# Kernel optimization log

Hardware: AMD Instinct MI355X
Metric: run time of the kernel (lower is better)

Reference implementation:

```python
import jax, jax.numpy as jnp
import numpy as np

B, S_ENC, T_DEC, I, H = 1024, 49, 25, 76, 2048  # S_ENC = source_seq_len - 1


def setup_inputs() -> dict:
    key = jax.random.key(0)
    ks = jax.random.split(key, 6)
    sc = 0.02
    return {
        "encoder_inputs": jax.random.normal(ks[0], (B, S_ENC, I), jnp.float32),
        "decoder_inputs": jax.random.normal(ks[1], (B, T_DEC, I), jnp.float32),
        "W_ih": jax.random.normal(ks[2], (3 * H, I), jnp.float32) * sc,
        "W_hh": jax.random.normal(ks[3], (3 * H, H), jnp.float32) * sc,
        "b_ih": jnp.zeros((3 * H,), jnp.float32),
        "b_hh": jnp.zeros((3 * H,), jnp.float32),
        "fc_w": jax.random.normal(ks[4], (I, H), jnp.float32) * sc,
        "fc_b": jnp.zeros((I,), jnp.float32),
    }


def gru_cell(x, h, W_ih, W_hh, b_ih, b_hh):
    # PyTorch GRUCell: gates stacked [r; z; n] along first axis of weights.
    gi = x @ W_ih.T + b_ih  # [B, 3H]
    gh = h @ W_hh.T + b_hh  # [B, 3H]
    i_r, i_z, i_n = jnp.split(gi, 3, axis=-1)
    h_r, h_z, h_n = jnp.split(gh, 3, axis=-1)
    r = jax.nn.sigmoid(i_r + h_r)
    z = jax.nn.sigmoid(i_z + h_z)
    n = jnp.tanh(i_n + r * h_n)
    return (1.0 - z) * n + z * h


def reference(encoder_inputs, decoder_inputs, W_ih, W_hh, b_ih, b_hh, fc_w, fc_b):
    # Dropout p=0.0 (and eval mode) -> identity; omitted.
    h0 = jnp.zeros((encoder_inputs.shape[0], H), encoder_inputs.dtype)
    enc = jnp.swapaxes(encoder_inputs, 0, 1)  # [S_ENC, B, I]

    def enc_step(h, x):
        return gru_cell(x, h, W_ih, W_hh, b_ih, b_hh), None

    h, _ = jax.lax.scan(enc_step, h0, enc)

    # Sampling-based decoding: only decoder_inputs[:, 0] is consumed; every
    # later step feeds back the previous output. Each step's input is detached.
    prev0 = decoder_inputs[:, 0, :]

    def dec_step(carry, _):
        h, prev = carry
        inp = jax.lax.stop_gradient(prev)  # inp.detach() in the torch code
        h_new = gru_cell(inp, h, W_ih, W_hh, b_ih, b_hh)
        out = inp + h_new @ fc_w.T + fc_b  # residual over fc1 projection
        return (h_new, out), out

    _, outs = jax.lax.scan(dec_step, (h, prev0), None, length=T_DEC)
    return jnp.swapaxes(outs, 0, 1)  # [B, T_DEC, I]
```

## Files before the change

### kernel.cpp

```cpp
#include <hip/hip_runtime.h>
#include <cstdint>
#include <cstddef>

#define DI __device__ __forceinline__

typedef __bf16 bf16x8 __attribute__((ext_vector_type(8)));
typedef float  f32x4  __attribute__((ext_vector_type(4)));
typedef unsigned short ushort_t;

constexpr int BATCH = 1024;
constexpr int HID   = 2048;
constexpr int IN    = 76;
constexpr int SENC  = 49;
constexpr int TDEC  = 25;
constexpr int KX    = 128;
constexpr int KP    = KX + HID;
constexpr int BK    = 64;
constexpr int KTT   = KP / BK;
constexpr int OSTR  = TDEC * IN;

DI unsigned short f2bf(float f) {
  union { float f; unsigned u; } v; v.f = f;
  unsigned u = v.u;
  return (unsigned short)((u + 0x7fffu + ((u >> 16) & 1u)) >> 16);
}

DI float bf2f(unsigned short h) {
  union { unsigned u; float f; } v; v.u = ((unsigned)h) << 16;
  return v.f;
}

DI f32x4 mfma16(bf16x8 a, bf16x8 b, f32x4 c) {
  return __builtin_amdgcn_mfma_f32_16x16x32_bf16(a, b, c, 0, 0, 0);
}

DI void gload_lds16(const void* g, void* l) {
  __builtin_amdgcn_global_load_lds((const __attribute__((address_space(1))) void*)g,
                                   (__attribute__((address_space(3))) void*)l,
                                   16, 0, 0);
}

DI float sigmoidf_(float x) { return 1.0f / (1.0f + __expf(-x)); }
DI float tanhf_(float x)    { return 1.0f - 2.0f / (1.0f + __expf(2.0f * x)); }


__global__ void pack_W(const float* __restrict__ Wih, const float* __restrict__ Whh,
                       ushort_t* __restrict__ Wp) {
  int idx = blockIdx.x * 256 + threadIdx.x;
  if (idx >= 6144 * KP) return;
  int n = idx / KP;
  int k = idx - n * KP;
  float v = 0.f;
  if (k < IN)        v = Wih[(size_t)n * IN + k];
  else if (k >= KX)  v = Whh[(size_t)n * HID + (k - KX)];
  Wp[idx] = f2bf(v);
}

__global__ void pack_xe(const float* __restrict__ enc, ushort_t* __restrict__ xe) {
  int idx = blockIdx.x * 256 + threadIdx.x;
  if (idx >= SENC * BATCH * KX) return;
  int t = idx >> 17;
  int rem = idx & 131071;
  int b = rem >> 7, k = rem & 127;
  float v = (k < IN) ? enc[(size_t)b * (SENC * IN) + t * IN + k] : 0.f;
  xe[idx] = f2bf(v);
}

__global__ void pack_xd0(const float* __restrict__ dec, ushort_t* __restrict__ xd) {
  int idx = blockIdx.x * 256 + threadIdx.x;
  if (idx >= BATCH * KX) return;
  int b = idx >> 7, k = idx & 127;
  float v = (k < IN) ? dec[(size_t)b * OSTR + k] : 0.f;
  xd[idx] = f2bf(v);
}

__global__ void pack_fc(const float* __restrict__ fcw, ushort_t* __restrict__ Wfc) {
  int idx = blockIdx.x * 256 + threadIdx.x;
  if (idx >= 80 * HID) return;
  int n = idx >> 11, k = idx & 2047;
  float v = (n < IN) ? fcw[(size_t)n * HID + k] : 0.f;
  Wfc[idx] = f2bf(v);
}

__global__ __launch_bounds__(256, 2) void gru_step_kernel(
    const ushort_t* __restrict__ x,
    const ushort_t* __restrict__ hbp,
    const ushort_t* __restrict__ Wp,
    const float*    __restrict__ b_ih,
    const float*    __restrict__ b_hh,
    ushort_t*       __restrict__ hbn)
{
  __shared__ ushort_t lds[2][(128 + 96) * BK];

  const int tid  = threadIdx.x;
  const int lane = tid & 63;
  const int wid  = tid >> 6;
  const int bid  = blockIdx.x;
  const int xcd   = bid & 7;
  const int idx   = bid >> 3;
  const int m_grp = idx & 7;
  const int n_grp = xcd + 8 * (idx >> 3);
  const int row0  = m_grp * 128;
  const int col0  = n_grp * 32;
  const int wm = wid >> 1;
  const int wn = wid & 1;

  const f32x4 Z4 = {0.f, 0.f, 0.f, 0.f};
  f32x4 accr[4], accz[4], accN[4], accin[4];
  #pragma unroll
  for (int a = 0; a < 4; ++a) { accr[a] = Z4; accz[a] = Z4; accN[a] = Z4; accin[a] = Z4; }

  const int srow  = lane >> 3;
  const int swcol = (((lane & 7) ^ (srow & 7)) << 3);

  const int lr  = lane & 15;
  const int bc  = (lane >> 4) * 16;
  const int ksw0 = ((bc)      ^ ((lane & 7) << 4)) >> 1;
  const int ksw1 = ((64 + bc) ^ ((lane & 7) << 4)) >> 1;

  auto stage = [&](int buf, int kt) {
    const ushort_t* asrc; int astr, ak0;
    if (kt < 2) { asrc = x;   astr = KX;  ak0 = kt * BK; }
    else        { asrc = hbp; astr = HID; ak0 = (kt - 2) * BK; }
    ushort_t* Lb = &lds[buf][0];
    #pragma unroll
    for (int c = 0; c < 4; ++c) {
      const int chunk = wid * 4 + c;
      const ushort_t* g = asrc + (size_t)(row0 + chunk * 8 + srow) * astr + ak0 + swcol;
      gload_lds16(g, Lb + chunk * 512);
    }
    const int wk0 = kt * BK;
    #pragma unroll
    for (int c = 0; c < 3; ++c) {
      const int chunk = wid * 3 + c;
      const int brow = chunk * 8 + srow;
      const int gg = brow >> 5, wi = brow & 31;
      const ushort_t* g = Wp + (size_t)(gg * HID + col0 + wi) * KP + wk0 + swcol;
      gload_lds16(g, Lb + 128 * BK + chunk * 512);
    }
  };

  auto readFrags = [&](const ushort_t* base, int ko, bf16x8 af[4], bf16x8 bg[3]) {
    #pragma unroll
    for (int fm = 0; fm < 4; ++fm)
      af[fm] = *reinterpret_cast<const bf16x8*>(&base[(wm * 64 + fm * 16 + lr) * BK + ko]);
    #pragma unroll
    for (int g = 0; g < 3; ++g)
      bg[g] = *reinterpret_cast<const bf16x8*>(
          &base[128 * BK + (g * 32 + wn * 16 + lr) * BK + ko]);
  };

  auto burst = [&](bf16x8 af[4], bf16x8 bg[3]) {
    __builtin_amdgcn_s_setprio(1);
    #pragma unroll
    for (int fm = 0; fm < 4; ++fm) {
      accr[fm] = mfma16(af[fm], bg[0], accr[fm]);
      accz[fm] = mfma16(af[fm], bg[1], accz[fm]);
      accN[fm] = mfma16(af[fm], bg[2], accN[fm]);
    }
    __builtin_amdgcn_s_setprio(0);
  };

  bf16x8 afA[4], bgA[3];
  bf16x8 afB[4], bgB[3];

  stage(0, 0);
  asm volatile("s_waitcnt vmcnt(0)" ::: "memory");
  __builtin_amdgcn_s_barrier();

  for (int kt = 0; kt < KTT; ++kt) {
    const ushort_t* base = &lds[kt & 1][0];
    if (kt + 1 < KTT) stage((kt + 1) & 1, kt + 1);
    readFrags(base, ksw0, afA, bgA);
    readFrags(base, ksw1, afB, bgB);
    burst(afA, bgA);
    burst(afB, bgB);

    if (kt == 1) {
      #pragma unroll
      for (int a = 0; a < 4; ++a) { accin[a] = accN[a]; accN[a] = Z4; }
    }

    if (kt + 1 < KTT) {
      asm volatile("s_waitcnt vmcnt(0)" ::: "memory");
      __builtin_amdgcn_s_barrier();
    }
  }

  const int lqb = (lane >> 4) * 4;
  const int j = col0 + wn * 16 + lr;
  const float br  = b_ih[j] + b_hh[j];
  const float bz  = b_ih[HID + j] + b_hh[HID + j];
  const float bin = b_ih[2 * HID + j];
  const float bhn = b_hh[2 * HID + j];
  #pragma unroll
  for (int fm = 0; fm < 4; ++fm) {
    #pragma unroll
    for (int q = 0; q < 4; ++q) {
      const int row = row0 + wm * 64 + fm * 16 + lqb + q;
      const size_t off = (size_t)row * HID + j;
      const float hp = bf2f(hbp[off]);
      const float rr = sigmoidf_(accr[fm][q] + br);
      const float zz = sigmoidf_(accz[fm][q] + bz);
      const float nn = tanhf_(accin[fm][q] + bin + rr * (accN[fm][q] + bhn));
      const float hv = (1.0f - zz) * nn + zz * hp;
      hbn[off] = f2bf(hv);
    }
  }
}

__global__ __launch_bounds__(256) void fc_kernel(
    const ushort_t* __restrict__ hb,
    const ushort_t* __restrict__ Wfc,
    const float*    __restrict__ fc_b,
    const float*    __restrict__ prev,
    float*          __restrict__ outp,
    ushort_t*       __restrict__ xd)
{
  __shared__ float red[4][16][80];
  const int tid = threadIdx.x, lane = tid & 63, wid = tid >> 6;
  const int r0 = blockIdx.x * 16;
  const int lr = lane & 15, lk = (lane >> 4) * 8;
  const f32x4 Z4 = {0.f, 0.f, 0.f, 0.f};
  f32x4 acc[5];
  #pragma unroll
  for (int f = 0; f < 5; ++f) acc[f] = Z4;
  const int kbase = wid * 512;
  #pragma unroll
  for (int ks = 0; ks < 16; ++ks) {
    const int k = kbase + ks * 32 + lk;
    bf16x8 a = *reinterpret_cast<const bf16x8*>(&hb[(size_t)(r0 + lr) * HID + k]);
    #pragma unroll
    for (int f = 0; f < 5; ++f) {
      bf16x8 b = *reinterpret_cast<const bf16x8*>(&Wfc[(size_t)(f * 16 + lr) * HID + k]);
      acc[f] = mfma16(a, b, acc[f]);
    }
  }
  #pragma unroll
  for (int f = 0; f < 5; ++f)
    #pragma unroll
    for (int q = 0; q < 4; ++q)
      red[wid][(lane >> 4) * 4 + q][f * 16 + lr] = acc[f][q];
  __syncthreads();

  const int rowi = tid >> 4;
  const int j0   = (tid & 15) * 8;
  const int b_   = r0 + rowi;
  #pragma unroll
  for (int jj = 0; jj < 8; ++jj) {
    const int j = j0 + jj;
    float ov = 0.f;
    if (j < IN) {
      float s = red[0][rowi][j] + red[1][rowi][j] + red[2][rowi][j] + red[3][rowi][j];
      ov = prev[(size_t)b_ * OSTR + j] + fc_b[j] + s;
      outp[(size_t)b_ * OSTR + j] = ov;
    }
    xd[b_ * KX + j] = f2bf(j < IN ? ov : 0.f);
  }
}

extern "C" void kernel_launch(void* const* d_in, const int* in_sizes, int n_in,
                              void* d_out, int out_size, void* d_ws, size_t ws_size,
                              hipStream_t stream) {
  const float* enc = (const float*)d_in[0];
  const float* dec = (const float*)d_in[1];
  const float* Wih = (const float*)d_in[2];
  const float* Whh = (const float*)d_in[3];
  const float* bih = (const float*)d_in[4];
  const float* bhh = (const float*)d_in[5];
  const float* fcw = (const float*)d_in[6];
  const float* fcb = (const float*)d_in[7];
  float* out = (float*)d_out;

  char* ws = (char*)d_ws;
  ushort_t* Wp  = (ushort_t*)ws;  ws += (size_t)6144 * KP * 2;
  ushort_t* xe  = (ushort_t*)ws;  ws += (size_t)SENC * BATCH * KX * 2;
  ushort_t* xd  = (ushort_t*)ws;  ws += (size_t)BATCH * KX * 2;
  ushort_t* Wfc = (ushort_t*)ws;  ws += (size_t)80 * HID * 2;
  ushort_t* hb0 = (ushort_t*)ws;  ws += (size_t)BATCH * HID * 2;
  ushort_t* hb1 = (ushort_t*)ws;  ws += (size_t)BATCH * HID * 2;
  ushort_t* hbp[2] = {hb0, hb1};

  pack_W  <<<(6144 * KP + 255) / 256, 256, 0, stream>>>(Wih, Whh, Wp);
  pack_xe <<<(SENC * BATCH * KX + 255) / 256, 256, 0, stream>>>(enc, xe);
  pack_xd0<<<(BATCH * KX + 255) / 256, 256, 0, stream>>>(dec, xd);
  pack_fc <<<(80 * HID + 255) / 256, 256, 0, stream>>>(fcw, Wfc);
  hipMemsetAsync(hb0, 0, (size_t)BATCH * HID * 2, stream);

  for (int s = 0; s < SENC + TDEC; ++s) {
    const ushort_t* xsrc = (s < SENC) ? (xe + (size_t)s * BATCH * KX) : xd;
    gru_step_kernel<<<512, 256, 0, stream>>>(xsrc, hbp[s & 1], Wp, bih, bhh,
                                             hbp[(s + 1) & 1]);
    if (s >= SENC) {
      const int t = s - SENC;
      const float* prev = (t == 0) ? dec : (out + (size_t)(t - 1) * IN);
      fc_kernel<<<64, 256, 0, stream>>>(hbp[(s + 1) & 1], Wfc, fcb, prev,
                                        out + (size_t)t * IN, xd);
    }
  }
}
```

Baseline: 2.583 ms.

## Load GRU activation operand directly into registers, stage only weights in LDS

The A operand (input and hidden-state rows) is now fetched from global memory straight into double-buffered registers one K-tile ahead, instead of being staged through LDS. Only the weight tile goes through LDS. This cuts the LDS footprint from two 224-row buffers to two 96-row buffers and removes the LDS round-trip for activations. The cost is higher VGPR pressure (two 8-fragment A buffers per lane), and the two waves sharing the same rows now each fetch them from global separately. The main loop is unrolled by two to ping-pong the register buffers.

```diff
diff --git a/kernel.cpp b/kernel.cpp
--- a/kernel.cpp
+++ b/kernel.cpp
@@ -90,7 +90,7 @@
     const float*    __restrict__ b_hh,
     ushort_t*       __restrict__ hbn)
 {
-  __shared__ ushort_t lds[2][(128 + 96) * BK];
+  __shared__ ushort_t lds[2][96 * BK];
 
   const int tid  = threadIdx.x;
   const int lane = tid & 63;
@@ -114,43 +114,43 @@
   const int swcol = (((lane & 7) ^ (srow & 7)) << 3);
 
   const int lr  = lane & 15;
-  const int bc  = (lane >> 4) * 16;
+  const int lhi = lane >> 4;
+  const int bc  = lhi * 16;
   const int ksw0 = ((bc)      ^ ((lane & 7) << 4)) >> 1;
   const int ksw1 = ((64 + bc) ^ ((lane & 7) << 4)) >> 1;
 
-  auto stage = [&](int buf, int kt) {
-    const ushort_t* asrc; int astr, ak0;
-    if (kt < 2) { asrc = x;   astr = KX;  ak0 = kt * BK; }
-    else        { asrc = hbp; astr = HID; ak0 = (kt - 2) * BK; }
+  auto stageB = [&](int buf, int kt) {
+    const int wk0 = kt * BK;
     ushort_t* Lb = &lds[buf][0];
-    #pragma unroll
-    for (int c = 0; c < 4; ++c) {
-      const int chunk = wid * 4 + c;
-      const ushort_t* g = asrc + (size_t)(row0 + chunk * 8 + srow) * astr + ak0 + swcol;
-      gload_lds16(g, Lb + chunk * 512);
-    }
-    const int wk0 = kt * BK;
     #pragma unroll
     for (int c = 0; c < 3; ++c) {
       const int chunk = wid * 3 + c;
       const int brow = chunk * 8 + srow;
       const int gg = brow >> 5, wi = brow & 31;
       const ushort_t* g = Wp + (size_t)(gg * HID + col0 + wi) * KP + wk0 + swcol;
-      gload_lds16(g, Lb + 128 * BK + chunk * 512);
-    }
-  };
-
-  auto readFrags = [&](const ushort_t* base, int ko, bf16x8 af[4], bf16x8 bg[3]) {
-    #pragma unroll
-    for (int fm = 0; fm < 4; ++fm)
-      af[fm] = *reinterpret_cast<const bf16x8*>(&base[(wm * 64 + fm * 16 + lr) * BK + ko]);
+      gload_lds16(g, Lb + chunk * 512);
+    }
+  };
+
+  auto loadA = [&](int kt, bf16x8 (&a)[8]) {
+    const ushort_t* asrc; int astr, ak0;
+    if (kt < 2) { asrc = x;   astr = KX;  ak0 = kt * BK; }
+    else        { asrc = hbp; astr = HID; ak0 = (kt - 2) * BK; }
+    #pragma unroll
+    for (int ks = 0; ks < 2; ++ks)
+      #pragma unroll
+      for (int fm = 0; fm < 4; ++fm)
+        a[ks * 4 + fm] = *reinterpret_cast<const bf16x8*>(
+            &asrc[(size_t)(row0 + wm * 64 + fm * 16 + lr) * astr + ak0 + ks * 32 + lhi * 8]);
+  };
+
+  auto readB = [&](const ushort_t* Lb, int ko, bf16x8 bg[3]) {
     #pragma unroll
     for (int g = 0; g < 3; ++g)
-      bg[g] = *reinterpret_cast<const bf16x8*>(
-          &base[128 * BK + (g * 32 + wn * 16 + lr) * BK + ko]);
-  };
-
-  auto burst = [&](bf16x8 af[4], bf16x8 bg[3]) {
+      bg[g] = *reinterpret_cast<const bf16x8*>(&Lb[(g * 32 + wn * 16 + lr) * BK + ko]);
+  };
+
+  auto burst = [&](const bf16x8* af, bf16x8 bg[3]) {
     __builtin_amdgcn_s_setprio(1);
     #pragma unroll
     for (int fm = 0; fm < 4; ++fm) {
@@ -161,33 +161,40 @@
     __builtin_amdgcn_s_setprio(0);
   };
 
-  bf16x8 afA[4], bgA[3];
-  bf16x8 afB[4], bgB[3];
-
-  stage(0, 0);
-  asm volatile("s_waitcnt vmcnt(0)" ::: "memory");
-  __builtin_amdgcn_s_barrier();
-
-  for (int kt = 0; kt < KTT; ++kt) {
-    const ushort_t* base = &lds[kt & 1][0];
-    if (kt + 1 < KTT) stage((kt + 1) & 1, kt + 1);
-    readFrags(base, ksw0, afA, bgA);
-    readFrags(base, ksw1, afB, bgB);
-    burst(afA, bgA);
-    burst(afB, bgB);
-
+  bf16x8 A0[8], A1[8];
+  bf16x8 bg0[3], bg1[3];
+
+  auto body = [&](int kt, bf16x8 (&aUse)[8], bf16x8 (&aPre)[8]) {
+    if (kt + 1 < KTT) {
+      loadA(kt + 1, aPre);
+      stageB((kt + 1) & 1, kt + 1);
+    }
+    const ushort_t* Lb = &lds[kt & 1][0];
+    readB(Lb, ksw0, bg0);
+    readB(Lb, ksw1, bg1);
+    burst(&aUse[0], bg0);
+    burst(&aUse[4], bg1);
     if (kt == 1) {
       #pragma unroll
       for (int a = 0; a < 4; ++a) { accin[a] = accN[a]; accN[a] = Z4; }
     }
-
     if (kt + 1 < KTT) {
       asm volatile("s_waitcnt vmcnt(0)" ::: "memory");
       __builtin_amdgcn_s_barrier();
     }
-  }
-
-  const int lqb = (lane >> 4) * 4;
+  };
+
+  loadA(0, A0);
+  stageB(0, 0);
+  asm volatile("s_waitcnt vmcnt(0)" ::: "memory");
+  __builtin_amdgcn_s_barrier();
+
+  for (int kt = 0; kt < KTT; kt += 2) {
+    body(kt,     A0, A1);
+    body(kt + 1, A1, A0);
+  }
+
+  const int lqb = lhi * 4;
   const int j = col0 + wn * 16 + lr;
   const float br  = b_ih[j] + b_hh[j];
   const float bz  = b_ih[HID + j] + b_hh[HID + j];
```

Result: slower. 5.853 ms (+126.6%).
